# Kernel tuning notes

Hardware: AMD Instinct MI355X
Metric: run time of the kernel (lower is better)

The kernel has to match this reference:

```python
import jax, jax.numpy as jnp
import numpy as np
import math

BLOCK = 4      # block_size
N_HEADS = 8
DIM = 512
COND = 512
B = 2
HWU = 32       # h = w = u
NN = 7         # 'cross' neighbors


def _layernorm(x, w, eps=1e-5):
    mu = x.mean(-1, keepdims=True)
    var = ((x - mu) ** 2).mean(-1, keepdims=True)
    return (x - mu) * jax.lax.rsqrt(var + eps) * w


def _modulate(x, shift, scale):
    return x * (1.0 + scale) + shift


def _rotate_half(x):
    x1, x2 = jnp.split(x, 2, axis=-1)
    return jnp.concatenate([-x2, x1], axis=-1)


def _rot(x, cos, sin):
    return x * cos + _rotate_half(x) * sin


def setup_inputs() -> dict:
    key = jax.random.key(0)
    ks = jax.random.split(key, 16)
    h = w = u = HWU
    S = h * w * u
    dh = DIM // N_HEADS
    P = BLOCK ** 3
    ib = HWU // BLOCK                       # blocks per axis = 8
    nb = ib ** 3                            # 512 blocks per batch

    x = jax.random.normal(ks[0], (B, S, DIM), jnp.float32)
    c = jax.random.normal(ks[1], (B, COND), jnp.float32)

    # proper rotary tables over P block-local positions
    inv = 1.0 / (10000.0 ** (np.arange(0, dh, 2, dtype=np.float32) / dh))
    f = np.arange(P, dtype=np.float32)[:, None] * inv[None, :]
    emb = np.concatenate([f, f], axis=-1)          # [P, dh]
    cos = jnp.asarray(np.cos(emb))[None, :, None, :]
    sin = jnp.asarray(np.sin(emb))[None, :, None, :]

    # neighbor indices (cross pattern) on the block grid, mirroring get_neighbor_indices
    grid = np.stack(np.meshgrid(np.arange(B), np.arange(ib), np.arange(ib), np.arange(ib), indexing='ij'), axis=-1)
    shifts = np.array([[0, 0, 0, 0], [0, 0, -1, 0], [0, -1, 0, 0], [0, 0, 0, -1],
                       [0, 0, 1, 0], [0, 1, 0, 0], [0, 0, 0, 1]])
    nbr = grid[..., None, :] + shifts[None, None, None, None, :, :]
    nbr[..., 1:] = np.clip(nbr[..., 1:], 0, ib - 1)
    flat = (nbr[..., 0] * ib * ib * ib + nbr[..., 1] * ib * ib
            + nbr[..., 2] * ib + nbr[..., 3]).reshape(B * nb, NN)
    # every other block is 'nonzero' -> Nsel = 512
    nonzero_blocks = np.arange(0, B * nb, 2, dtype=np.int64)
    nonzero_blocks_neighbor = flat[nonzero_blocks].reshape(-1).astype(np.int64)

    s = 0.02
    params = dict(
        norm1_w=jnp.ones((DIM,), jnp.float32),
        qkv_w=s * jax.random.normal(ks[2], (3 * DIM, DIM), jnp.float32),
        out_w=s * jax.random.normal(ks[3], (DIM, DIM), jnp.float32),
        norm2_w=jnp.ones((DIM,), jnp.float32),
        mlp_w1=s * jax.random.normal(ks[4], (4 * DIM, DIM), jnp.float32),
        mlp_b1=jnp.zeros((4 * DIM,), jnp.float32),
        mlp_w2=s * jax.random.normal(ks[5], (DIM, 4 * DIM), jnp.float32),
        mlp_b2=jnp.zeros((DIM,), jnp.float32),
        adaln_w=s * jax.random.normal(ks[6], (6 * DIM, COND), jnp.float32),
        adaln_b=jnp.zeros((6 * DIM,), jnp.float32),
        kv_empty=s * jax.random.normal(ks[7], (1, P, 2 * DIM), jnp.float32),
    )
    return dict(x=x, c=c, cos_q=cos, sin_q=sin, cos_k=cos, sin_k=sin,
                nonzero_blocks=jnp.asarray(nonzero_blocks),
                nonzero_blocks_neighbor=jnp.asarray(nonzero_blocks_neighbor),
                h=h, w=w, u=u, **params)


def reference(x, c, cos_q, sin_q, cos_k, sin_k, nonzero_blocks, nonzero_blocks_neighbor,
              h, w, u, norm1_w, qkv_w, out_w, norm2_w, mlp_w1, mlp_b1, mlp_w2, mlp_b2,
              adaln_w, adaln_b, kv_empty):
    Bx, S, D = x.shape
    bs = BLOCK
    ix, iy, iz = h // bs, w // bs, u // bs
    nb = ix * iy * iz
    P = bs ** 3
    dh = D // N_HEADS
    Nsel = nonzero_blocks.shape[0]

    def transform(t):
        t = t.reshape(Bx, ix, bs, iy, bs, iz, bs, D)
        return t.transpose(0, 1, 3, 5, 2, 4, 6, 7).reshape(Bx, nb, P, D)

    def inverse_transform(t):
        t = t.reshape(Bx, ix, iy, iz, bs, bs, bs, D)
        return t.transpose(0, 1, 4, 2, 5, 3, 6, 7).reshape(Bx, S, D)

    mods = (c @ adaln_w.T + adaln_b)[:, None, :]         # [B,1,6D]
    shift_msa, scale_msa, gate_msa, shift_mlp, scale_mlp, gate_mlp = jnp.split(mods, 6, axis=-1)

    x_skip = x
    xm = _modulate(_layernorm(x, norm1_w), shift_msa, scale_msa)
    xb = transform(xm).reshape(Bx * nb, P, D)
    x_sel = xb[nonzero_blocks]                            # [Nsel,P,D]

    qkv = x_sel @ qkv_w.T                                 # [Nsel,P,3D]
    q, k, v = jnp.split(qkv, 3, axis=-1)
    k_e, v_e = jnp.split(kv_empty, 2, axis=-1)            # [1,P,D]
    k_full = jnp.broadcast_to(k_e, (Bx * nb, P, D)).at[nonzero_blocks].set(k)
    v_full = jnp.broadcast_to(v_e, (Bx * nb, P, D)).at[nonzero_blocks].set(v)
    kn = k_full[nonzero_blocks_neighbor]                  # [Nsel*NN,P,D]
    vn = v_full[nonzero_blocks_neighbor]

    qh = _rot(q.reshape(Nsel, P, N_HEADS, dh), cos_q, sin_q)
    kh = _rot(kn.reshape(Nsel * NN, P, N_HEADS, dh), cos_k, sin_k)
    kh = kh.reshape(Nsel, NN * P, N_HEADS, dh)
    vh = vn.reshape(Nsel, NN * P, N_HEADS, dh)

    scores = jnp.einsum('bqhd,bkhd->bhqk', qh, kh) / math.sqrt(dh)
    attn = jax.nn.softmax(scores, axis=-1)
    out = jnp.einsum('bhqk,bkhd->bqhd', attn, vh).reshape(Nsel, P, D)

    xz = jnp.zeros((Bx * nb, P, D), out.dtype).at[nonzero_blocks].set(out)
    x_attn = inverse_transform(xz.reshape(Bx, nb, P, D))
    x1 = x_skip + gate_msa * (x_attn @ out_w.T)

    x2 = _modulate(_layernorm(x1, norm2_w), shift_mlp, scale_mlp)
    mlp = jax.nn.gelu(x2 @ mlp_w1.T + mlp_b1, approximate=True) @ mlp_w2.T + mlp_b2
    return x1 + gate_mlp * mlp
```

## Files before the change

### kernel.cpp

```cpp
#include <hip/hip_runtime.h>
#include <cstdint>
#include <cstddef>

typedef unsigned short u16;
typedef __attribute__((ext_vector_type(8))) __bf16 bf16x8;
typedef __attribute__((ext_vector_type(4))) float f32x4;

typedef __attribute__((address_space(1))) const void GAS;
typedef __attribute__((address_space(3))) void LAS;

__device__ __forceinline__ void gld_lds16(const void* g, void* l) {
  __builtin_amdgcn_global_load_lds((GAS*)g, (LAS*)l, 16, 0, 0);
}

__device__ __forceinline__ u16 f2bf(float f) {
  union { float f; unsigned u; } x; x.f = f;
  unsigned r = x.u + 0x7FFFu + ((x.u >> 16) & 1u);
  return (u16)(r >> 16);
}
__device__ __forceinline__ float bf2f(u16 s) {
  union { unsigned u; float f; } x; x.u = ((unsigned)s) << 16;
  return x.f;
}
__device__ __forceinline__ f32x4 mfma16(bf16x8 a, bf16x8 b, f32x4 c) {
  return __builtin_amdgcn_mfma_f32_16x16x32_bf16(a, b, c, 0, 0, 0);
}


__global__ void selmap_k(const int* __restrict__ nzb, int* __restrict__ map) {
  int t = threadIdx.x;
  map[t] = -1;
  __syncthreads();
  if (t < 512) map[nzb[t]] = t;
}

__global__ __launch_bounds__(256) void castw_k(const float* __restrict__ in,
                                               u16* __restrict__ out, int n4) {
  int i = blockIdx.x * 256 + threadIdx.x;
  if (i >= n4) return;
  float4 v = ((const float4*)in)[i];
  u16 o[4] = {f2bf(v.x), f2bf(v.y), f2bf(v.z), f2bf(v.w)};
  ((uint2*)out)[i] = *(uint2*)o;
}

__global__ __launch_bounds__(256) void adaln_k(const float* __restrict__ c,
    const float* __restrict__ w, const float* __restrict__ b, float* __restrict__ mods) {
  int j = blockIdx.x * 256 + threadIdx.x;
  int bt = blockIdx.y;
  const float4* cr = (const float4*)(c + bt * 512);
  const float4* wr = (const float4*)(w + (size_t)j * 512);
  float s = 0.f;
  #pragma unroll 4
  for (int k = 0; k < 128; ++k) {
    float4 a = wr[k], q = cr[k];
    s += a.x * q.x + a.y * q.y + a.z * q.z + a.w * q.w;
  }
  mods[bt * 3072 + j] = s + b[j];
}

__global__ __launch_bounds__(256) void kvempty_k(const float* __restrict__ kve,
    const float* __restrict__ cT, const float* __restrict__ sT,
    u16* __restrict__ kempty, u16* __restrict__ vTempty) {
  int T = blockIdx.x * 256 + threadIdx.x;
  int h = T >> 12, p = (T >> 6) & 63, d = T & 63;
  float kv = kve[p * 1024 + h * 64 + d];
  float pv = kve[p * 1024 + h * 64 + (d ^ 32)];
  float cs = cT[p * 64 + d], sn = sT[p * 64 + d];
  float r = kv * cs + ((d < 32) ? -pv : pv) * sn;
  kempty[(h * 64 + p) * 64 + d] = f2bf(r);
  vTempty[(h * 64 + d) * 64 + p] = f2bf(kve[p * 1024 + 512 + h * 64 + d]);
}


__global__ __launch_bounds__(256) void ln1_k(const float* __restrict__ x,
    const float* __restrict__ nw, const float* __restrict__ mods,
    const int* __restrict__ nzb, u16* __restrict__ xm) {
  int row = blockIdx.x * 4 + (threadIdx.x >> 6);
  int t = threadIdx.x & 63;
  int sel = row >> 6, p = row & 63;
  int g = nzb[sel];
  int bt = g >> 9, blk = g & 511;
  int s = (blk >> 6) * 4096 + (p >> 4) * 1024 + ((blk >> 3) & 7) * 128
        + ((p >> 2) & 3) * 32 + (blk & 7) * 4 + (p & 3);
  const float* src = x + ((size_t)bt * 32768 + s) * 512;
  int d0 = t * 8;
  float4 a = *(const float4*)(src + d0);
  float4 b = *(const float4*)(src + d0 + 4);
  float v[8] = {a.x, a.y, a.z, a.w, b.x, b.y, b.z, b.w};
  float sum = 0.f, sq = 0.f;
  #pragma unroll
  for (int j = 0; j < 8; ++j) { sum += v[j]; sq += v[j] * v[j]; }
  #pragma unroll
  for (int m = 1; m < 64; m <<= 1) {
    sum += __shfl_xor(sum, m, 64);
    sq  += __shfl_xor(sq, m, 64);
  }
  float mean = sum * (1.f / 512.f);
  float var = sq * (1.f / 512.f) - mean * mean;
  float rstd = rsqrtf(var + 1e-5f);
  const float* mb = mods + bt * 3072;
  u16 o[8];
  #pragma unroll
  for (int j = 0; j < 8; ++j) {
    int d = d0 + j;
    float xn = (v[j] - mean) * rstd * nw[d];
    o[j] = f2bf(xn * (1.f + mb[512 + d]) + mb[d]);
  }
  *(uint4*)(xm + (size_t)row * 512 + d0) = *(uint4*)o;
}


template <int EPI>
__global__ __launch_bounds__(256, 4) void gemm128(const u16* __restrict__ A,
    const u16* __restrict__ W, int M, int N, int K, void* __restrict__ outp,
    const float* __restrict__ bias, const u16* __restrict__ x1,
    const float* __restrict__ mods, int NB,
    const float* __restrict__ cq, const float* __restrict__ sq,
    const float* __restrict__ ck, const float* __restrict__ sk,
    u16* __restrict__ qb, u16* __restrict__ kb, u16* __restrict__ vb) {
  __shared__ u16 L[2][8192];
  const int nwg = gridDim.x;
  const int cpx = nwg >> 3;
  const int tile = ((int)blockIdx.x & 7) * cpx + ((int)blockIdx.x >> 3);
  const int bm = (tile / NB) * 128, bn = (tile % NB) * 128;
  const int tid = threadIdx.x;
  const int w = tid >> 6, l = tid & 63, lr = l & 15, lg = l >> 4;
  const int wr = w >> 1, wc = w & 1;

  const int s0 = tid, s1 = 256 + tid;
  const int rA0 = s0 >> 2, j0 = (s0 & 3) ^ ((s0 >> 3) & 3);
  const int rA1 = s1 >> 2, j1 = (s1 & 3) ^ ((s1 >> 3) & 3);
  const u16* gA0 = A + (size_t)(bm + rA0) * K + j0 * 8;
  const u16* gA1 = A + (size_t)(bm + rA1) * K + j1 * 8;
  const u16* gB0 = W + (size_t)(bn + rA0) * K + j0 * 8;
  const u16* gB1 = W + (size_t)(bn + rA1) * K + j1 * 8;

  f32x4 acc[4][4];
  #pragma unroll
  for (int i = 0; i < 4; ++i)
    #pragma unroll
    for (int j = 0; j < 4; ++j) acc[i][j] = (f32x4){0.f, 0.f, 0.f, 0.f};

  auto STAGE = [&](int kt, int buf) {
    u16* lb = &L[buf][0];
    gld_lds16(gA0 + (size_t)kt * 32, lb + s0 * 8);
    gld_lds16(gA1 + (size_t)kt * 32, lb + s1 * 8);
    gld_lds16(gB0 + (size_t)kt * 32, lb + 4096 + s0 * 8);
    gld_lds16(gB1 + (size_t)kt * 32, lb + 4096 + s1 * 8);
  };
  auto COMPUTE = [&](int buf) {
    const u16* base = &L[buf][0];
    bf16x8 bfr[4];
    #pragma unroll
    for (int nf = 0; nf < 4; ++nf) {
      int rB = wc * 64 + nf * 16 + lr;
      bfr[nf] = *(const bf16x8*)(base + 4096 + rB * 32 + ((lg ^ ((rB >> 1) & 3)) << 3));
    }
    __builtin_amdgcn_s_setprio(1);
    #pragma unroll
    for (int mf = 0; mf < 4; ++mf) {
      int rA = wr * 64 + mf * 16 + lr;
      bf16x8 a = *(const bf16x8*)(base + rA * 32 + ((lg ^ ((rA >> 1) & 3)) << 3));
      #pragma unroll
      for (int nf = 0; nf < 4; ++nf)
        acc[mf][nf] = mfma16(a, bfr[nf], acc[mf][nf]);
    }
    __builtin_amdgcn_s_setprio(0);
  };

  const int NT = K >> 5;
  STAGE(0, 0);
  for (int t = 0; t < NT; ++t) {
    if (t + 1 < NT) {
      STAGE(t + 1, (t + 1) & 1);
      asm volatile("s_waitcnt vmcnt(4)" ::: "memory");
    } else {
      asm volatile("s_waitcnt vmcnt(0)" ::: "memory");
    }
    __builtin_amdgcn_sched_barrier(0);
    __builtin_amdgcn_s_barrier();
    asm volatile("" ::: "memory");
    COMPUTE(t & 1);
    asm volatile("" ::: "memory");
    __builtin_amdgcn_s_barrier();
    __builtin_amdgcn_sched_barrier(0);
  }

  const int row0 = bm + wr * 64, col0 = bn + wc * 64;
  #pragma unroll
  for (int mf = 0; mf < 4; ++mf) {
    #pragma unroll
    for (int nf = 0; nf < 4; ++nf) {
      #pragma unroll
      for (int j = 0; j < 4; ++j) {
        int row = row0 + mf * 16 + lg * 4 + j;
        int col = col0 + nf * 16 + lr;
        float v = acc[mf][nf][j];
        if constexpr (EPI == 0) {
          ((u16*)outp)[(size_t)row * N + col] = f2bf(v);
        } else if constexpr (EPI == 2) {
          v += bias[col];
          float z = 1.5957691216057308f * (v + 0.044715f * v * v * v);
          float t = 1.f - 2.f / (1.f + __expf(z));
          ((u16*)outp)[(size_t)row * N + col] = f2bf(0.5f * v * (1.f + t));
        } else if constexpr (EPI == 3) {
          v += bias[col];
          int bt = row >> 15;
          float gate = mods[bt * 3072 + 2560 + col];
          ((float*)outp)[(size_t)row * 512 + col] =
              bf2f(x1[(size_t)row * 512 + col]) + gate * v;
        } else {
          int sel = row >> 6, p = row & 63;
          if (col < 1024) {
            int isk = col >= 512;
            int h = (col >> 6) & 7, d64 = col & 63;
            int lower = (d64 < 32);
            float pv = acc[mf][nf ^ 2][j];
            const float* cT = isk ? ck : cq;
            const float* sT = isk ? sk : sq;
            float r = v * cT[p * 64 + d64] + (lower ? -pv : pv) * sT[p * 64 + d64];
            if (!isk) r *= 0.125f;
            u16* dst = (isk ? kb : qb) + (((size_t)sel * 8 + h) * 64 + p) * 64 + d64;
            *dst = f2bf(r);
          } else {
            vb[(size_t)row * 512 + (col - 1024)] = f2bf(v);
          }
        }
      }
    }
  }
}


__global__ __launch_bounds__(256) void vtrans_k(const u16* __restrict__ vbuf,
                                                u16* __restrict__ vT) {
  __shared__ u16 tb[64 * 65];
  int sel = blockIdx.x >> 3, h = blockIdx.x & 7;
  int tid = threadIdx.x;
  int p = tid >> 2, q16 = (tid & 3) * 16;
  const u16* src = vbuf + (size_t)(sel * 64 + p) * 512 + h * 64 + q16;
  u16 ld[16];
  *(uint4*)&ld[0] = *(const uint4*)src;
  *(uint4*)&ld[8] = *(const uint4*)(src + 8);
  #pragma unroll
  for (int j = 0; j < 16; ++j) tb[p * 65 + q16 + j] = ld[j];
  __syncthreads();
  int d = tid >> 2, po = (tid & 3) * 16;
  u16 o[16];
  #pragma unroll
  for (int j = 0; j < 16; ++j) o[j] = tb[(po + j) * 65 + d];
  u16* dst = vT + (((size_t)sel * 8 + h) * 64 + d) * 64 + po;
  *(uint4*)dst = *(uint4*)&o[0];
  *(uint4*)(dst + 8) = *(uint4*)&o[8];
}


__global__ __launch_bounds__(256, 4) void attn_k(const u16* __restrict__ qbuf,
    const u16* __restrict__ kfull, const u16* __restrict__ vT,
    const u16* __restrict__ kempty, const u16* __restrict__ vTempty,
    const int* __restrict__ nbrs, const int* __restrict__ selmap,
    u16* __restrict__ attnout) {
  __shared__ u16 Pl[4][16][72];
  int bid = blockIdx.x;
  int swz = (bid & 7) * 512 + (bid >> 3);
  int sel = swz >> 3, h = swz & 7;
  int tid = threadIdx.x;
  int w = tid >> 6, l = tid & 63, lr = l & 15, lg = l >> 4;

  int mmv[7];
  #pragma unroll
  for (int n = 0; n < 7; ++n) mmv[n] = selmap[nbrs[sel * 7 + n]];

  const u16* qg = qbuf + (((size_t)sel * 8 + h) * 64 + w * 16) * 64;
  bf16x8 qf0 = *(const bf16x8*)(qg + lr * 64 + lg * 8);
  bf16x8 qf1 = *(const bf16x8*)(qg + lr * 64 + 32 + lg * 8);
  size_t hoff = (size_t)h * 4096;

  f32x4 o[4];
  float mrun[4], lrun[4];
  #pragma unroll
  for (int ct = 0; ct < 4; ++ct) o[ct] = (f32x4){0.f, 0.f, 0.f, 0.f};
  #pragma unroll
  for (int r = 0; r < 4; ++r) { mrun[r] = -1e30f; lrun[r] = 0.f; }

  #pragma unroll
  for (int n = 0; n < 7; ++n) {
    const u16* kp = (mmv[n] >= 0) ? kfull + (size_t)mmv[n] * 32768 + hoff
                                  : kempty + hoff;
    const u16* vp = (mmv[n] >= 0) ? vT + (size_t)mmv[n] * 32768 + hoff
                                  : vTempty + hoff;
    f32x4 s4[4];
    #pragma unroll
    for (int ct = 0; ct < 4; ++ct) {
      bf16x8 b0 = *(const bf16x8*)(kp + (ct * 16 + lr) * 64 + lg * 8);
      bf16x8 b1 = *(const bf16x8*)(kp + (ct * 16 + lr) * 64 + 32 + lg * 8);
      f32x4 z = (f32x4){0.f, 0.f, 0.f, 0.f};
      z = mfma16(qf0, b0, z);
      z = mfma16(qf1, b1, z);
      s4[ct] = z;
    }
    float rmax[4], sc[4], rs[4];
    #pragma unroll
    for (int r = 0; r < 4; ++r)
      rmax[r] = fmaxf(fmaxf(s4[0][r], s4[1][r]), fmaxf(s4[2][r], s4[3][r]));
    #pragma unroll
    for (int r = 0; r < 4; ++r) {
      #pragma unroll
      for (int ms = 1; ms < 16; ms <<= 1)
        rmax[r] = fmaxf(rmax[r], __shfl_xor(rmax[r], ms, 64));
      float mn = fmaxf(mrun[r], rmax[r]);
      sc[r] = __expf(mrun[r] - mn);
      mrun[r] = mn;
      rs[r] = 0.f;
    }
    #pragma unroll
    for (int ct = 0; ct < 4; ++ct)
      #pragma unroll
      for (int r = 0; r < 4; ++r) {
        float e = __expf(s4[ct][r] - mrun[r]);
        s4[ct][r] = e;
        rs[r] += e;
      }
    #pragma unroll
    for (int r = 0; r < 4; ++r) {
      #pragma unroll
      for (int ms = 1; ms < 16; ms <<= 1) rs[r] += __shfl_xor(rs[r], ms, 64);
      lrun[r] = lrun[r] * sc[r] + rs[r];
    }
    #pragma unroll
    for (int ct = 0; ct < 4; ++ct)
      #pragma unroll
      for (int r = 0; r < 4; ++r) o[ct][r] *= sc[r];
    #pragma unroll
    for (int ct = 0; ct < 4; ++ct)
      #pragma unroll
      for (int r = 0; r < 4; ++r)
        Pl[w][lg * 4 + r][ct * 16 + lr] = f2bf(s4[ct][r]);
    asm volatile("s_waitcnt lgkmcnt(0)" ::: "memory");
    __builtin_amdgcn_sched_barrier(0);
    bf16x8 pa0 = *(const bf16x8*)&Pl[w][lr][lg * 8];
    bf16x8 pa1 = *(const bf16x8*)&Pl[w][lr][32 + lg * 8];
    #pragma unroll
    for (int ct = 0; ct < 4; ++ct) {
      bf16x8 v0 = *(const bf16x8*)(vp + (ct * 16 + lr) * 64 + lg * 8);
      bf16x8 v1 = *(const bf16x8*)(vp + (ct * 16 + lr) * 64 + 32 + lg * 8);
      o[ct] = mfma16(pa0, v0, o[ct]);
      o[ct] = mfma16(pa1, v1, o[ct]);
    }
    __builtin_amdgcn_sched_barrier(0);
  }

  float inv[4];
  #pragma unroll
  for (int r = 0; r < 4; ++r) inv[r] = 1.f / lrun[r];
  #pragma unroll
  for (int ct = 0; ct < 4; ++ct)
    #pragma unroll
    for (int r = 0; r < 4; ++r) {
      int p = w * 16 + lg * 4 + r;
      int d = ct * 16 + lr;
      attnout[((size_t)sel * 64 + p) * 512 + h * 64 + d] = f2bf(o[ct][r] * inv[r]);
    }
}


__global__ __launch_bounds__(256) void x1ln2_k(const float* __restrict__ x,
    const u16* __restrict__ opout, const int* __restrict__ selmap,
    const float* __restrict__ mods, const float* __restrict__ nw,
    u16* __restrict__ x1, u16* __restrict__ x2) {
  int row = blockIdx.x * 4 + (threadIdx.x >> 6);
  int t = threadIdx.x & 63;
  int bt = row >> 15, s = row & 32767;
  int i1 = s >> 12, p1 = (s >> 10) & 3, i2 = (s >> 7) & 7,
      p2 = (s >> 5) & 3, i3 = (s >> 2) & 7, p3 = s & 3;
  int blk = (((i1 << 3) | i2) << 3) | i3;
  int m = selmap[(bt << 9) | blk];
  int d0 = t * 8;
  const float* src = x + (size_t)row * 512 + d0;
  float4 a = *(const float4*)src;
  float4 b = *(const float4*)(src + 4);
  float v[8] = {a.x, a.y, a.z, a.w, b.x, b.y, b.z, b.w};
  const float* mb = mods + bt * 3072;
  if (m >= 0) {
    int p = (p1 << 4) | (p2 << 2) | p3;
    const u16* op = opout + ((size_t)m * 64 + p) * 512 + d0;
    u16 oh[8];
    *(uint4*)oh = *(const uint4*)op;
    #pragma unroll
    for (int j = 0; j < 8; ++j) v[j] += mb[1024 + d0 + j] * bf2f(oh[j]);
  }
  u16 o1[8];
  #pragma unroll
  for (int j = 0; j < 8; ++j) o1[j] = f2bf(v[j]);
  *(uint4*)(x1 + (size_t)row * 512 + d0) = *(uint4*)o1;
  float sum = 0.f, sq = 0.f;
  #pragma unroll
  for (int j = 0; j < 8; ++j) { sum += v[j]; sq += v[j] * v[j]; }
  #pragma unroll
  for (int mm = 1; mm < 64; mm <<= 1) {
    sum += __shfl_xor(sum, mm, 64);
    sq  += __shfl_xor(sq, mm, 64);
  }
  float mean = sum * (1.f / 512.f);
  float var = sq * (1.f / 512.f) - mean * mean;
  float rstd = rsqrtf(var + 1e-5f);
  u16 o[8];
  #pragma unroll
  for (int j = 0; j < 8; ++j) {
    int d = d0 + j;
    float xn = (v[j] - mean) * rstd * nw[d];
    o[j] = f2bf(xn * (1.f + mb[2048 + d]) + mb[1536 + d]);
  }
  *(uint4*)(x2 + (size_t)row * 512 + d0) = *(uint4*)o;
}


extern "C" void kernel_launch(void* const* d_in, const int* in_sizes, int n_in,
                              void* d_out, int out_size, void* d_ws, size_t ws_size,
                              hipStream_t stream) {
  const float* x    = (const float*)d_in[0];
  const float* c    = (const float*)d_in[1];
  const float* cosq = (const float*)d_in[2];
  const float* sinq = (const float*)d_in[3];
  const float* cosk = (const float*)d_in[4];
  const float* sink = (const float*)d_in[5];
  const int* nzb    = (const int*)d_in[6];
  const int* nbrs   = (const int*)d_in[7];
  const float* norm1_w = (const float*)d_in[11];
  const float* qkv_w   = (const float*)d_in[12];
  const float* out_w   = (const float*)d_in[13];
  const float* norm2_w = (const float*)d_in[14];
  const float* mlp_w1  = (const float*)d_in[15];
  const float* mlp_b1  = (const float*)d_in[16];
  const float* mlp_w2  = (const float*)d_in[17];
  const float* mlp_b2  = (const float*)d_in[18];
  const float* adaln_w = (const float*)d_in[19];
  const float* adaln_b = (const float*)d_in[20];
  const float* kv_e    = (const float*)d_in[21];
  float* outp = (float*)d_out;
  char* ws = (char*)d_ws;

  const size_t MB = 1024ull * 1024ull;
  u16*   vbuf    = (u16*)(ws + 0);
  u16*   opout   = (u16*)(ws + 0);
  u16*   hidden  = (u16*)(ws + 0);
  u16*   xm      = (u16*)(ws + 96 * MB);
  u16*   attnout = (u16*)(ws + 96 * MB);
  u16*   qb      = (u16*)(ws + 128 * MB);
  u16*   kf      = (u16*)(ws + 160 * MB);
  u16*   vT      = (u16*)(ws + 192 * MB);
  u16*   x1      = (u16*)(ws + 256 * MB);
  u16*   x2      = (u16*)(ws + 320 * MB);
  char*  S0      = ws + 384 * MB;
  float* mods    = (float*)(S0);
  int*   selmap  = (int*)(S0 + 0x8000);
  u16*   kempty  = (u16*)(S0 + 0x10000);
  u16*   vTempty = (u16*)(S0 + 0x20000);
  u16*   qkvw_bf = (u16*)(S0 + 0x30000);
  u16*   outw_bf = qkvw_bf + (size_t)1536 * 512;
  u16*   w1_bf   = outw_bf + (size_t)512 * 512;
  u16*   w2_bf   = w1_bf + (size_t)2048 * 512;

  selmap_k<<<1, 1024, 0, stream>>>(nzb, selmap);
  adaln_k<<<dim3(12, 2), 256, 0, stream>>>(c, adaln_w, adaln_b, mods);
  castw_k<<<768, 256, 0, stream>>>(qkv_w, qkvw_bf, 1536 * 512 / 4);
  castw_k<<<256, 256, 0, stream>>>(out_w, outw_bf, 512 * 512 / 4);
  castw_k<<<1024, 256, 0, stream>>>(mlp_w1, w1_bf, 2048 * 512 / 4);
  castw_k<<<1024, 256, 0, stream>>>(mlp_w2, w2_bf, 512 * 2048 / 4);
  kvempty_k<<<128, 256, 0, stream>>>(kv_e, cosk, sink, kempty, vTempty);

  ln1_k<<<8192, 256, 0, stream>>>(x, norm1_w, mods, nzb, xm);

  gemm128<4><<<3072, 256, 0, stream>>>(xm, qkvw_bf, 32768, 1536, 512, nullptr,
                                       nullptr, nullptr, nullptr, 12,
                                       cosq, sinq, cosk, sink, qb, kf, vbuf);
  vtrans_k<<<4096, 256, 0, stream>>>(vbuf, vT);

  attn_k<<<4096, 256, 0, stream>>>(qb, kf, vT, kempty, vTempty, nbrs, selmap, attnout);

  gemm128<0><<<1024, 256, 0, stream>>>(attnout, outw_bf, 32768, 512, 512, opout,
                                       nullptr, nullptr, nullptr, 4,
                                       nullptr, nullptr, nullptr, nullptr,
                                       nullptr, nullptr, nullptr);

  x1ln2_k<<<16384, 256, 0, stream>>>(x, opout, selmap, mods, norm2_w, x1, x2);

  gemm128<2><<<8192, 256, 0, stream>>>(x2, w1_bf, 65536, 2048, 512, hidden,
                                       mlp_b1, nullptr, nullptr, 16,
                                       nullptr, nullptr, nullptr, nullptr,
                                       nullptr, nullptr, nullptr);
  gemm128<3><<<2048, 256, 0, stream>>>(hidden, w2_bf, 65536, 512, 2048, outp,
                                       mlp_b2, x1, mods, 4,
                                       nullptr, nullptr, nullptr, nullptr,
                                       nullptr, nullptr, nullptr);
}
```

Baseline: 973.3 us.

## Make GEMMs persistent over tile chunks and process two rows per wave in LN kernels

The GEMM kernel now launches a fixed grid of 1024 workgroups, and each one walks CH consecutive output tiles in M-major order. The K-loop prefetch runs across tile boundaries, so the next tile's loads overlap the current tile's epilogue, and the column-major tile order improves reuse of weight tiles across neighbouring workgroups. The two layernorm kernels now process two rows per wavefront, loading the weight and modulation vectors once for both rows. This cuts launch and tail overhead and adds pipelining across tiles, but it relies on K/32 being a power of two and grid*CH matching the tile count exactly.

```diff
diff --git a/kernel.cpp b/kernel.cpp
--- a/kernel.cpp
+++ b/kernel.cpp
@@ -75,38 +75,50 @@
 __global__ __launch_bounds__(256) void ln1_k(const float* __restrict__ x,
     const float* __restrict__ nw, const float* __restrict__ mods,
     const int* __restrict__ nzb, u16* __restrict__ xm) {
-  int row = blockIdx.x * 4 + (threadIdx.x >> 6);
+  int row0 = blockIdx.x * 8 + (threadIdx.x >> 6) * 2;
   int t = threadIdx.x & 63;
-  int sel = row >> 6, p = row & 63;
+  int sel = row0 >> 6, p = row0 & 63;
   int g = nzb[sel];
   int bt = g >> 9, blk = g & 511;
   int s = (blk >> 6) * 4096 + (p >> 4) * 1024 + ((blk >> 3) & 7) * 128
         + ((p >> 2) & 3) * 32 + (blk & 7) * 4 + (p & 3);
   const float* src = x + ((size_t)bt * 32768 + s) * 512;
   int d0 = t * 8;
-  float4 a = *(const float4*)(src + d0);
-  float4 b = *(const float4*)(src + d0 + 4);
-  float v[8] = {a.x, a.y, a.z, a.w, b.x, b.y, b.z, b.w};
-  float sum = 0.f, sq = 0.f;
-  #pragma unroll
-  for (int j = 0; j < 8; ++j) { sum += v[j]; sq += v[j] * v[j]; }
-  #pragma unroll
-  for (int m = 1; m < 64; m <<= 1) {
-    sum += __shfl_xor(sum, m, 64);
-    sq  += __shfl_xor(sq, m, 64);
-  }
-  float mean = sum * (1.f / 512.f);
-  float var = sq * (1.f / 512.f) - mean * mean;
-  float rstd = rsqrtf(var + 1e-5f);
+  float v[2][8];
+  #pragma unroll
+  for (int rr = 0; rr < 2; ++rr) {
+    float4 a = *(const float4*)(src + rr * 512 + d0);
+    float4 b = *(const float4*)(src + rr * 512 + d0 + 4);
+    v[rr][0] = a.x; v[rr][1] = a.y; v[rr][2] = a.z; v[rr][3] = a.w;
+    v[rr][4] = b.x; v[rr][5] = b.y; v[rr][6] = b.z; v[rr][7] = b.w;
+  }
   const float* mb = mods + bt * 3072;
-  u16 o[8];
+  float wv[8], sh[8], sc[8];
   #pragma unroll
   for (int j = 0; j < 8; ++j) {
-    int d = d0 + j;
-    float xn = (v[j] - mean) * rstd * nw[d];
-    o[j] = f2bf(xn * (1.f + mb[512 + d]) + mb[d]);
-  }
-  *(uint4*)(xm + (size_t)row * 512 + d0) = *(uint4*)o;
+    wv[j] = nw[d0 + j]; sh[j] = mb[d0 + j]; sc[j] = mb[512 + d0 + j];
+  }
+  #pragma unroll
+  for (int rr = 0; rr < 2; ++rr) {
+    float sum = 0.f, sq = 0.f;
+    #pragma unroll
+    for (int j = 0; j < 8; ++j) { sum += v[rr][j]; sq += v[rr][j] * v[rr][j]; }
+    #pragma unroll
+    for (int m = 1; m < 64; m <<= 1) {
+      sum += __shfl_xor(sum, m, 64);
+      sq  += __shfl_xor(sq, m, 64);
+    }
+    float mean = sum * (1.f / 512.f);
+    float var = sq * (1.f / 512.f) - mean * mean;
+    float rstd = rsqrtf(var + 1e-5f);
+    u16 o[8];
+    #pragma unroll
+    for (int j = 0; j < 8; ++j) {
+      float xn = (v[rr][j] - mean) * rstd * wv[j];
+      o[j] = f2bf(xn * (1.f + sc[j]) + sh[j]);
+    }
+    *(uint4*)(xm + (size_t)(row0 + rr) * 512 + d0) = *(uint4*)o;
+  }
 }
 
 
@@ -114,15 +126,15 @@
 __global__ __launch_bounds__(256, 4) void gemm128(const u16* __restrict__ A,
     const u16* __restrict__ W, int M, int N, int K, void* __restrict__ outp,
     const float* __restrict__ bias, const u16* __restrict__ x1,
-    const float* __restrict__ mods, int NB,
+    const float* __restrict__ mods, int NMTsh, int CH,
     const float* __restrict__ cq, const float* __restrict__ sq,
     const float* __restrict__ ck, const float* __restrict__ sk,
     u16* __restrict__ qb, u16* __restrict__ kb, u16* __restrict__ vb) {
   __shared__ u16 L[2][8192];
   const int nwg = gridDim.x;
   const int cpx = nwg >> 3;
-  const int tile = ((int)blockIdx.x & 7) * cpx + ((int)blockIdx.x >> 3);
-  const int bm = (tile / NB) * 128, bn = (tile % NB) * 128;
+  const int gch = ((int)blockIdx.x & 7) * cpx + ((int)blockIdx.x >> 3);
+  const int NMTm1 = (1 << NMTsh) - 1;
   const int tid = threadIdx.x;
   const int w = tid >> 6, l = tid & 63, lr = l & 15, lg = l >> 4;
   const int wr = w >> 1, wc = w & 1;
@@ -130,10 +142,17 @@
   const int s0 = tid, s1 = 256 + tid;
   const int rA0 = s0 >> 2, j0 = (s0 & 3) ^ ((s0 >> 3) & 3);
   const int rA1 = s1 >> 2, j1 = (s1 & 3) ^ ((s1 >> 3) & 3);
-  const u16* gA0 = A + (size_t)(bm + rA0) * K + j0 * 8;
-  const u16* gA1 = A + (size_t)(bm + rA1) * K + j1 * 8;
-  const u16* gB0 = W + (size_t)(bn + rA0) * K + j0 * 8;
-  const u16* gB1 = W + (size_t)(bn + rA1) * K + j1 * 8;
+
+  const u16 *gA0, *gA1, *gB0, *gB1;
+  int pbm, pbn;
+  auto setstage = [&](int T) {
+    pbm = (T & NMTm1) * 128;
+    pbn = (T >> NMTsh) * 128;
+    gA0 = A + (size_t)(pbm + rA0) * K + j0 * 8;
+    gA1 = A + (size_t)(pbm + rA1) * K + j1 * 8;
+    gB0 = W + (size_t)(pbn + rA0) * K + j0 * 8;
+    gB1 = W + (size_t)(pbn + rA1) * K + j1 * 8;
+  };
 
   f32x4 acc[4][4];
   #pragma unroll
@@ -168,11 +187,67 @@
     __builtin_amdgcn_s_setprio(0);
   };
 
-  const int NT = K >> 5;
+  auto EPILOGUE = [&](int bm, int bn) {
+    const int row0 = bm + wr * 64, col0 = bn + wc * 64;
+    #pragma unroll
+    for (int mf = 0; mf < 4; ++mf) {
+      #pragma unroll
+      for (int nf = 0; nf < 4; ++nf) {
+        #pragma unroll
+        for (int j = 0; j < 4; ++j) {
+          int row = row0 + mf * 16 + lg * 4 + j;
+          int col = col0 + nf * 16 + lr;
+          float v = acc[mf][nf][j];
+          if constexpr (EPI == 0) {
+            ((u16*)outp)[(size_t)row * N + col] = f2bf(v);
+          } else if constexpr (EPI == 2) {
+            v += bias[col];
+            float z = 1.5957691216057308f * (v + 0.044715f * v * v * v);
+            float t = 1.f - 2.f / (1.f + __expf(z));
+            ((u16*)outp)[(size_t)row * N + col] = f2bf(0.5f * v * (1.f + t));
+          } else if constexpr (EPI == 3) {
+            v += bias[col];
+            int bt = row >> 15;
+            float gate = mods[bt * 3072 + 2560 + col];
+            ((float*)outp)[(size_t)row * 512 + col] =
+                bf2f(x1[(size_t)row * 512 + col]) + gate * v;
+          } else {
+            int sel = row >> 6, p = row & 63;
+            if (col < 1024) {
+              int isk = col >= 512;
+              int h = (col >> 6) & 7, d64 = col & 63;
+              int lower = (d64 < 32);
+              float pv = acc[mf][nf ^ 2][j];
+              const float* cT = isk ? ck : cq;
+              const float* sT = isk ? sk : sq;
+              float r = v * cT[p * 64 + d64] + (lower ? -pv : pv) * sT[p * 64 + d64];
+              if (!isk) r *= 0.125f;
+              u16* dst = (isk ? kb : qb) + (((size_t)sel * 8 + h) * 64 + p) * 64 + d64;
+              *dst = f2bf(r);
+            } else {
+              vb[(size_t)row * 512 + (col - 1024)] = f2bf(v);
+            }
+          }
+        }
+      }
+    }
+    #pragma unroll
+    for (int i = 0; i < 4; ++i)
+      #pragma unroll
+      for (int j = 0; j < 4; ++j) acc[i][j] = (f32x4){0.f, 0.f, 0.f, 0.f};
+  };
+
+  const int NT = K >> 5, NTm1 = NT - 1;
+  int Tn = gch * CH;
+  setstage(Tn);
+  int bmC = pbm, bnC = pbn;
   STAGE(0, 0);
-  for (int t = 0; t < NT; ++t) {
-    if (t + 1 < NT) {
-      STAGE(t + 1, (t + 1) & 1);
+  const int total = CH * NT;
+  for (int s = 0; s < total; ++s) {
+    if (s + 1 < total) {
+      int t1 = (s + 1) & NTm1;
+      if (t1 == 0) { ++Tn; setstage(Tn); }
+      STAGE(t1, (s + 1) & 1);
       asm volatile("s_waitcnt vmcnt(4)" ::: "memory");
     } else {
       asm volatile("s_waitcnt vmcnt(0)" ::: "memory");
@@ -180,53 +255,13 @@
     __builtin_amdgcn_sched_barrier(0);
     __builtin_amdgcn_s_barrier();
     asm volatile("" ::: "memory");
-    COMPUTE(t & 1);
+    COMPUTE(s & 1);
     asm volatile("" ::: "memory");
     __builtin_amdgcn_s_barrier();
     __builtin_amdgcn_sched_barrier(0);
-  }
-
-  const int row0 = bm + wr * 64, col0 = bn + wc * 64;
-  #pragma unroll
-  for (int mf = 0; mf < 4; ++mf) {
-    #pragma unroll
-    for (int nf = 0; nf < 4; ++nf) {
-      #pragma unroll
-      for (int j = 0; j < 4; ++j) {
-        int row = row0 + mf * 16 + lg * 4 + j;
-        int col = col0 + nf * 16 + lr;
-        float v = acc[mf][nf][j];
-        if constexpr (EPI == 0) {
-          ((u16*)outp)[(size_t)row * N + col] = f2bf(v);
-        } else if constexpr (EPI == 2) {
-          v += bias[col];
-          float z = 1.5957691216057308f * (v + 0.044715f * v * v * v);
-          float t = 1.f - 2.f / (1.f + __expf(z));
-          ((u16*)outp)[(size_t)row * N + col] = f2bf(0.5f * v * (1.f + t));
-        } else if constexpr (EPI == 3) {
-          v += bias[col];
-          int bt = row >> 15;
-          float gate = mods[bt * 3072 + 2560 + col];
-          ((float*)outp)[(size_t)row * 512 + col] =
-              bf2f(x1[(size_t)row * 512 + col]) + gate * v;
-        } else {
-          int sel = row >> 6, p = row & 63;
-          if (col < 1024) {
-            int isk = col >= 512;
-            int h = (col >> 6) & 7, d64 = col & 63;
-            int lower = (d64 < 32);
-            float pv = acc[mf][nf ^ 2][j];
-            const float* cT = isk ? ck : cq;
-            const float* sT = isk ? sk : sq;
-            float r = v * cT[p * 64 + d64] + (lower ? -pv : pv) * sT[p * 64 + d64];
-            if (!isk) r *= 0.125f;
-            u16* dst = (isk ? kb : qb) + (((size_t)sel * 8 + h) * 64 + p) * 64 + d64;
-            *dst = f2bf(r);
-          } else {
-            vb[(size_t)row * 512 + (col - 1024)] = f2bf(v);
-          }
-        }
-      }
+    if (((s + 1) & NTm1) == 0) {
+      EPILOGUE(bmC, bnC);
+      bmC = pbm; bnC = pbn;
     }
   }
 }
@@ -368,50 +403,66 @@
     const u16* __restrict__ opout, const int* __restrict__ selmap,
     const float* __restrict__ mods, const float* __restrict__ nw,
     u16* __restrict__ x1, u16* __restrict__ x2) {
-  int row = blockIdx.x * 4 + (threadIdx.x >> 6);
+  int row0 = blockIdx.x * 8 + (threadIdx.x >> 6) * 2;
   int t = threadIdx.x & 63;
-  int bt = row >> 15, s = row & 32767;
+  int bt = row0 >> 15, s = row0 & 32767;
   int i1 = s >> 12, p1 = (s >> 10) & 3, i2 = (s >> 7) & 7,
       p2 = (s >> 5) & 3, i3 = (s >> 2) & 7, p3 = s & 3;
   int blk = (((i1 << 3) | i2) << 3) | i3;
   int m = selmap[(bt << 9) | blk];
+  int p0 = (p1 << 4) | (p2 << 2) | p3;
   int d0 = t * 8;
-  const float* src = x + (size_t)row * 512 + d0;
-  float4 a = *(const float4*)src;
-  float4 b = *(const float4*)(src + 4);
-  float v[8] = {a.x, a.y, a.z, a.w, b.x, b.y, b.z, b.w};
+  const float* src = x + (size_t)row0 * 512 + d0;
+  float v[2][8];
+  #pragma unroll
+  for (int rr = 0; rr < 2; ++rr) {
+    float4 a = *(const float4*)(src + rr * 512);
+    float4 b = *(const float4*)(src + rr * 512 + 4);
+    v[rr][0] = a.x; v[rr][1] = a.y; v[rr][2] = a.z; v[rr][3] = a.w;
+    v[rr][4] = b.x; v[rr][5] = b.y; v[rr][6] = b.z; v[rr][7] = b.w;
+  }
   const float* mb = mods + bt * 3072;
+  float gm[8], sh2[8], sc2[8], wv[8];
+  #pragma unroll
+  for (int j = 0; j < 8; ++j) {
+    gm[j] = mb[1024 + d0 + j]; sh2[j] = mb[1536 + d0 + j];
+    sc2[j] = mb[2048 + d0 + j]; wv[j] = nw[d0 + j];
+  }
   if (m >= 0) {
-    int p = (p1 << 4) | (p2 << 2) | p3;
-    const u16* op = opout + ((size_t)m * 64 + p) * 512 + d0;
-    u16 oh[8];
-    *(uint4*)oh = *(const uint4*)op;
-    #pragma unroll
-    for (int j = 0; j < 8; ++j) v[j] += mb[1024 + d0 + j] * bf2f(oh[j]);
-  }
-  u16 o1[8];
-  #pragma unroll
-  for (int j = 0; j < 8; ++j) o1[j] = f2bf(v[j]);
-  *(uint4*)(x1 + (size_t)row * 512 + d0) = *(uint4*)o1;
-  float sum = 0.f, sq = 0.f;
-  #pragma unroll
-  for (int j = 0; j < 8; ++j) { sum += v[j]; sq += v[j] * v[j]; }
-  #pragma unroll
-  for (int mm = 1; mm < 64; mm <<= 1) {
-    sum += __shfl_xor(sum, mm, 64);
-    sq  += __shfl_xor(sq, mm, 64);
-  }
-  float mean = sum * (1.f / 512.f);
-  float var = sq * (1.f / 512.f) - mean * mean;
-  float rstd = rsqrtf(var + 1e-5f);
-  u16 o[8];
-  #pragma unroll
-  for (int j = 0; j < 8; ++j) {
-    int d = d0 + j;
-    float xn = (v[j] - mean) * rstd * nw[d];
-    o[j] = f2bf(xn * (1.f + mb[2048 + d]) + mb[1536 + d]);
-  }
-  *(uint4*)(x2 + (size_t)row * 512 + d0) = *(uint4*)o;
+    const u16* op = opout + ((size_t)m * 64 + p0) * 512 + d0;
+    #pragma unroll
+    for (int rr = 0; rr < 2; ++rr) {
+      u16 oh[8];
+      *(uint4*)oh = *(const uint4*)(op + rr * 512);
+      #pragma unroll
+      for (int j = 0; j < 8; ++j) v[rr][j] += gm[j] * bf2f(oh[j]);
+    }
+  }
+  #pragma unroll
+  for (int rr = 0; rr < 2; ++rr) {
+    u16 o1[8];
+    #pragma unroll
+    for (int j = 0; j < 8; ++j) o1[j] = f2bf(v[rr][j]);
+    *(uint4*)(x1 + (size_t)(row0 + rr) * 512 + d0) = *(uint4*)o1;
+    float sum = 0.f, sq = 0.f;
+    #pragma unroll
+    for (int j = 0; j < 8; ++j) { sum += v[rr][j]; sq += v[rr][j] * v[rr][j]; }
+    #pragma unroll
+    for (int mm = 1; mm < 64; mm <<= 1) {
+      sum += __shfl_xor(sum, mm, 64);
+      sq  += __shfl_xor(sq, mm, 64);
+    }
+    float mean = sum * (1.f / 512.f);
+    float var = sq * (1.f / 512.f) - mean * mean;
+    float rstd = rsqrtf(var + 1e-5f);
+    u16 o[8];
+    #pragma unroll
+    for (int j = 0; j < 8; ++j) {
+      float xn = (v[rr][j] - mean) * rstd * wv[j];
+      o[j] = f2bf(xn * (1.f + sc2[j]) + sh2[j]);
+    }
+    *(uint4*)(x2 + (size_t)(row0 + rr) * 512 + d0) = *(uint4*)o;
+  }
 }
 
 
@@ -469,28 +520,28 @@
   castw_k<<<1024, 256, 0, stream>>>(mlp_w2, w2_bf, 512 * 2048 / 4);
   kvempty_k<<<128, 256, 0, stream>>>(kv_e, cosk, sink, kempty, vTempty);
 
-  ln1_k<<<8192, 256, 0, stream>>>(x, norm1_w, mods, nzb, xm);
-
-  gemm128<4><<<3072, 256, 0, stream>>>(xm, qkvw_bf, 32768, 1536, 512, nullptr,
-                                       nullptr, nullptr, nullptr, 12,
+  ln1_k<<<4096, 256, 0, stream>>>(x, norm1_w, mods, nzb, xm);
+
+  gemm128<4><<<1024, 256, 0, stream>>>(xm, qkvw_bf, 32768, 1536, 512, nullptr,
+                                       nullptr, nullptr, nullptr, 8, 3,
                                        cosq, sinq, cosk, sink, qb, kf, vbuf);
   vtrans_k<<<4096, 256, 0, stream>>>(vbuf, vT);
 
   attn_k<<<4096, 256, 0, stream>>>(qb, kf, vT, kempty, vTempty, nbrs, selmap, attnout);
 
   gemm128<0><<<1024, 256, 0, stream>>>(attnout, outw_bf, 32768, 512, 512, opout,
-                                       nullptr, nullptr, nullptr, 4,
+                                       nullptr, nullptr, nullptr, 8, 1,
                                        nullptr, nullptr, nullptr, nullptr,
                                        nullptr, nullptr, nullptr);
 
-  x1ln2_k<<<16384, 256, 0, stream>>>(x, opout, selmap, mods, norm2_w, x1, x2);
-
-  gemm128<2><<<8192, 256, 0, stream>>>(x2, w1_bf, 65536, 2048, 512, hidden,
-                                       mlp_b1, nullptr, nullptr, 16,
+  x1ln2_k<<<8192, 256, 0, stream>>>(x, opout, selmap, mods, norm2_w, x1, x2);
+
+  gemm128<2><<<1024, 256, 0, stream>>>(x2, w1_bf, 65536, 2048, 512, hidden,
+                                       mlp_b1, nullptr, nullptr, 9, 8,
                                        nullptr, nullptr, nullptr, nullptr,
                                        nullptr, nullptr, nullptr);
-  gemm128<3><<<2048, 256, 0, stream>>>(hidden, w2_bf, 65536, 512, 2048, outp,
-                                       mlp_b2, x1, mods, 4,
+  gemm128<3><<<1024, 256, 0, stream>>>(hidden, w2_bf, 65536, 512, 2048, outp,
+                                       mlp_b2, x1, mods, 9, 2,
                                        nullptr, nullptr, nullptr, nullptr,
                                        nullptr, nullptr, nullptr);
 }
```

Result: slower. 1.035 ms (+6.3%).
